# Kernel optimization log

Measured on AMD Instinct MI355X. Metric: run time of the kernel, lower is better.

## Reference

```python
import jax, jax.numpy as jnp
import numpy as np
from math import factorial

# ---- static configuration (matches init_kwargs) ----
IRREPS_IN1 = [(32, 0, 1), (32, 1, -1), (32, 2, 1)]   # (mul, l, parity)
IRREPS_SH  = [(1, 0, 1), (1, 1, -1), (1, 2, 1)]
IRREPS_OUT = [(32, 0, 1), (32, 1, -1), (32, 2, 1)]
NUM_BASIS = 10
HIDDEN = 16
CUTOFF = 4.0
P_ENV = 6  # dimenet envelope_exponent (5) + 1

# ---- real Wigner 3j (Clebsch-Gordan in real SH basis), computed once in numpy ----
def _su2_cg(j1, j2, j3, m1, m2, m3):
    if m3 != m1 + m2:
        return 0.0
    f = factorial
    vmin = max(-j1 + j2 + m3, -j1 + m1, 0)
    vmax = min(j2 + j3 + m1, j3 - j1 + j2, j3 + m3)
    c = (f(2*j3+1) * f(j3+j1-j2) * f(j3-j1+j2) * f(j1+j2-j3) / f(j1+j2+j3+1)
         * f(j3+m3) * f(j3-m3) / (f(j1+m1) * f(j1-m1) * f(j2+m2) * f(j2-m2))) ** 0.5
    s = 0.0
    for v in range(vmin, vmax + 1):
        s += (-1)**(v + j2 + m2) * f(j2+j3+m1-v) * f(j1-m1+v) / (
             f(v) * f(j3-j1+j2-v) * f(j3+m3-v) * f(v+j1-j2-m3))
    return c * s

def _q(l):  # real -> complex SH change of basis
    q = np.zeros((2*l+1, 2*l+1), dtype=complex)
    for m in range(-l, 0):
        q[l+m, l+abs(m)] = 2**-0.5
        q[l+m, l-abs(m)] = -1j * 2**-0.5
    q[l, l] = 1.0
    for m in range(1, l+1):
        q[l+m, l+abs(m)] = (-1)**m * 2**-0.5
        q[l+m, l-abs(m)] = 1j * (-1)**m * 2**-0.5
    return (-1j)**l * q

def _wigner_3j(l1, l2, l3):
    csu2 = np.array([[[ _su2_cg(l1, l2, l3, m1, m2, m3)
                       for m3 in range(-l3, l3+1)]
                      for m2 in range(-l2, l2+1)]
                     for m1 in range(-l1, l1+1)], dtype=complex)
    c = np.einsum('ij,kl,mn,ikm->jln', _q(l1), _q(l2), np.conj(_q(l3)), csu2)
    c = np.real(c)
    n = np.linalg.norm(c)
    return c / n if n > 0 else c

def _slices(irreps):
    s, off = [], 0
    for mul, l, p in irreps:
        d = mul * (2*l + 1)
        s.append((off, off + d))
        off += d
    return s, off

SL1, DIM_IN1 = _slices(IRREPS_IN1)
SL2, DIM_SH = _slices(IRREPS_SH)
SL3, DIM_OUT = _slices(IRREPS_OUT)

_raw = []
for i1, (m1, l1, p1) in enumerate(IRREPS_IN1):
    for i2, (m2, l2, p2) in enumerate(IRREPS_SH):
        for i3, (m3, l3, p3) in enumerate(IRREPS_OUT):
            if p1 * p2 == p3 and abs(l1 - l2) <= l3 <= l1 + l2:
                _raw.append((i1, i2, i3))

_fan = {}
for i1, i2, i3 in _raw:  # path_normalization='element': fan-in per output slot
    _fan[i3] = _fan.get(i3, 0) + IRREPS_IN1[i1][0] * IRREPS_SH[i2][0]

INSTR = []
WEIGHT_NUMEL = 0
for i1, i2, i3 in _raw:
    m1, l1, _ = IRREPS_IN1[i1]
    m2, l2, _ = IRREPS_SH[i2]
    m3, l3, _ = IRREPS_OUT[i3]
    pw = ((2*l3 + 1) / _fan[i3]) ** 0.5  # irrep_normalization='component'
    C = _wigner_3j(l1, l2, l3).astype(np.float32)
    INSTR.append((i1, i2, i3, m1, l1, m2, l2, m3, l3, WEIGHT_NUMEL, pw, C))
    WEIGHT_NUMEL += m1 * m2 * m3

# ---- radial network: Bessel basis (with dimenet envelope) -> Linear -> SiLU -> Linear ----
def _radial(distance, freq, W1, b1, W2, b2):
    d = distance[:, 0]                      # squeeze(-1) -> [E]
    x = (d / CUTOFF)[:, None]               # [E, 1]
    p = P_ENV
    a = -(p + 1) * (p + 2) / 2.0
    b = float(p * (p + 2))
    c = -p * (p + 1) / 2.0
    env = (1.0 / x + a * x**(p-1) + b * x**p + c * x**(p+1)) * (x < 1.0).astype(x.dtype)
    basis = env * jnp.sin(freq * x)         # [E, NUM_BASIS]
    h = jax.nn.silu(basis @ W1 + b1)
    return h @ W2 + b2                      # [E, WEIGHT_NUMEL]

# ---- fully connected tensor product (uvw, external per-edge weights) ----
def _tp(x, sh, weights):
    E = x.shape[0]
    acc = [jnp.zeros((E, m, 2*l + 1), x.dtype) for m, l, _ in IRREPS_OUT]
    for (i1, i2, i3, m1, l1, m2, l2, m3, l3, woff, pw, C) in INSTR:
        a, b = SL1[i1]; xb = x[:, a:b].reshape(E, m1, 2*l1 + 1)
        a, b = SL2[i2]; sb = sh[:, a:b].reshape(E, m2, 2*l2 + 1)
        w = weights[:, woff:woff + m1*m2*m3].reshape(E, m1, m2, m3)
        Cj = jnp.asarray(C)
        acc[i3] = acc[i3] + pw * jnp.einsum('euvw,ijk,eui,evj->ewk', w, Cj, xb, sb)
    return jnp.concatenate([a.reshape(E, -1) for a in acc], axis=1)


def setup_inputs() -> dict:
    key = jax.random.key(0)
    ks = jax.random.split(key, 6)
    E = 16384
    x = jax.random.normal(ks[0], (E, DIM_IN1), jnp.float32)
    rel_pos_sh = jax.random.normal(ks[1], (E, DIM_SH), jnp.float32)
    # distances strictly inside (0, cutoff) so envelope 1/x and mask are benign
    distance = 0.25 + 3.5 * jax.random.uniform(ks[2], (E, 1), jnp.float32)
    freq = jnp.pi * jnp.arange(1, NUM_BASIS + 1, dtype=jnp.float32)
    W1 = 0.4 * jax.random.normal(ks[3], (NUM_BASIS, HIDDEN), jnp.float32)
    b1 = jnp.zeros((HIDDEN,), jnp.float32)
    W2 = 0.1 * jax.random.normal(ks[4], (HIDDEN, WEIGHT_NUMEL), jnp.float32)
    b2 = jnp.zeros((WEIGHT_NUMEL,), jnp.float32)
    return {"x": x, "rel_pos_sh": rel_pos_sh, "distance": distance,
            "freq": freq, "W1": W1, "b1": b1, "W2": W2, "b2": b2}


def reference(x, rel_pos_sh, distance, freq, W1, b1, W2, b2):
    weights = _radial(distance, freq, W1, b1, W2, b2)
    return _tp(x, rel_pos_sh, weights)
```

## Files before the change

### kernel.cpp

```cpp
#include <hip/hip_runtime.h>
#include <cmath>
#include <complex>
#include <cstring>
#include <algorithm>

#define DIM_IN  288
#define DIM_SHD 9
#define NB      10
#define NH      16
#define EPB     16
#define BLOCK   256
#define NINSTR  11
#define XSTR    292
#define ZSTR    164
#define W2B_ELEMS (NINSTR * 32 * 32 * 32)

#define OFF_XO 0
#define OFF_Z  4672
#define OFF_SH 9920
#define POOLSZ 10112

typedef __attribute__((ext_vector_type(8))) short  short8b;
typedef __attribute__((ext_vector_type(4))) float  f32x4;

__device__ float g_C[NINSTR][125];

__device__ __forceinline__ unsigned short f2bf(float f) {
  unsigned int u = __float_as_uint(f);
  unsigned int r = (u + 0x7fffu + ((u >> 16) & 1u)) >> 16;
  return (unsigned short)r;
}

__global__ __launch_bounds__(256) void prep_w2(const float* __restrict__ W2,
                                               const float* __restrict__ b2,
                                               unsigned short* __restrict__ W2b) {
  int gid = blockIdx.x * 256 + threadIdx.x;
  if (gid < W2B_ELEMS) {
    int c = gid >> 5, t = gid & 31;
    float v = (t < 16) ? W2[(size_t)t * 11264 + c] : (t == 16 ? b2[c] : 0.0f);
    W2b[gid] = f2bf(v);
  }
}

template<int INS,int D1,int D2,int D3,int OFF1,int OFF2>
__device__ __forceinline__ void z_phase(
    int tid, const float* __restrict__ s_x,
    const float* __restrict__ s_sh, float* __restrict__ zdst)
{
  const float* __restrict__ Cp = g_C[INS];
  #pragma unroll
  for (int s = 0; s < 2; ++s) {
    int id = tid + s * BLOCK;
    int e = id >> 5, u = id & 31;
    const float* xe = s_x + e * XSTR + OFF1 + u * D1;
    float zk[D3];
    #pragma unroll
    for (int k = 0; k < D3; ++k) zk[k] = 0.f;
    #pragma unroll
    for (int i = 0; i < D1; ++i) {
      float xv = xe[i];
      #pragma unroll
      for (int j = 0; j < D2; ++j) {
        float pr = xv * s_sh[e * 12 + OFF2 + j];
        #pragma unroll
        for (int k = 0; k < D3; ++k)
          zk[k] = fmaf(Cp[(i * D2 + j) * D3 + k], pr, zk[k]);
      }
    }
    #pragma unroll
    for (int k = 0; k < D3; ++k) zdst[e * ZSTR + k * 32 + u] = zk[k];
  }
}

template<int INS,int D3,int SB>
__device__ __forceinline__ void contract(
    int ls, int lq, int a_wt, int b_uh, int my_e,
    const unsigned short* __restrict__ W2b,
    const float* __restrict__ zbuf, short8b hB, float (&acc)[4][9])
{
  const unsigned short* Ap =
      W2b + ((size_t)(INS * 32 + b_uh * 16) * 32 + a_wt * 16 + ls) * 32 + lq * 8;
  const float* zb = zbuf + my_e * ZSTR + b_uh * 16;
  const f32x4 zero4 = {0.f, 0.f, 0.f, 0.f};

  short8b Ra = *(const short8b*)(Ap);
  f32x4 w_cur = __builtin_amdgcn_mfma_f32_16x16x32_bf16(Ra, hB, zero4, 0, 0, 0);
  short8b Rb = *(const short8b*)(Ap + 1024);

  #pragma unroll
  for (int c = 0; c < 4; ++c) {
    float4 zq[D3];
    #pragma unroll
    for (int k = 0; k < D3; ++k)
      zq[k] = *(const float4*)(zb + k * 32 + c * 4);
    #pragma unroll
    for (int i = 0; i < 4; ++i) {
      const int g = c * 4 + i;
      f32x4 w_next;
      if (g < 15) {
        w_next = __builtin_amdgcn_mfma_f32_16x16x32_bf16(Rb, hB, zero4, 0, 0, 0);
        if (g + 2 < 16) Rb = *(const short8b*)(Ap + (size_t)(g + 2) * 1024);
      }
      #pragma unroll
      for (int k = 0; k < D3; ++k) {
        const float zz = (i == 0) ? zq[k].x : (i == 1) ? zq[k].y
                       : (i == 2) ? zq[k].z : zq[k].w;
        acc[0][SB + k] = fmaf(w_cur[0], zz, acc[0][SB + k]);
        acc[1][SB + k] = fmaf(w_cur[1], zz, acc[1][SB + k]);
        acc[2][SB + k] = fmaf(w_cur[2], zz, acc[2][SB + k]);
        acc[3][SB + k] = fmaf(w_cur[3], zz, acc[3][SB + k]);
      }
      if (g < 15) w_cur = w_next;
    }
  }
}

__global__ __launch_bounds__(BLOCK, 2) void conv_kernel(
    const float* __restrict__ xg, const float* __restrict__ shg,
    const float* __restrict__ dist, const float* __restrict__ freq,
    const float* __restrict__ W1, const float* __restrict__ b1,
    const unsigned short* __restrict__ W2b,
    float* __restrict__ out)
{
  __shared__ float s_pool[POOLSZ];
  float* s_xo = s_pool + OFF_XO;
  float* s_z0 = s_pool + OFF_Z;
  float* s_z1 = s_pool + OFF_Z + EPB * ZSTR;
  float* s_sh = s_pool + OFF_SH;
  float* s_basis = s_z1;
  unsigned short* s_hb = (unsigned short*)(s_z1 + 160);

  const int tid = threadIdx.x;
  const int e0 = blockIdx.x * EPB;
  const int l  = tid & 63;
  const int ls = l & 15;
  const int lq = l >> 4;
  const int wid = tid >> 6;
  const int a_wt = wid >> 1;
  const int b_uh = wid & 1;
  const int my_e = ls;

  for (int i4 = tid; i4 < EPB * 72; i4 += BLOCK) {
    int e = i4 / 72, r = i4 - e * 72;
    *(float4*)(s_xo + e * XSTR + r * 4) =
        *(const float4*)(xg + (size_t)(e0 + e) * DIM_IN + r * 4);
  }
  if (tid < EPB * DIM_SHD) {
    int e = tid / DIM_SHD, c = tid - (tid / DIM_SHD) * DIM_SHD;
    s_sh[e * 12 + c] = shg[(size_t)(e0 + e) * DIM_SHD + c];
  }
  if (tid < EPB * NB) {
    int e = tid / NB, n = tid - (tid / NB) * NB;
    float d  = dist[e0 + e];
    float xv = d * 0.25f;
    float x2 = xv * xv, x4 = x2 * x2, x5 = x4 * xv;
    float env = 1.0f / xv + x5 * fmaf(xv, fmaf(xv, -21.0f, 48.0f), -28.0f);
    env = (xv < 1.0f) ? env : 0.0f;
    s_basis[e * NB + n] = env * sinf(freq[n] * xv);
  }
  __syncthreads();

  {
    int e = tid >> 4, t = tid & 15;
    float v = b1[t];
    #pragma unroll
    for (int n = 0; n < NB; ++n) v = fmaf(s_basis[e * NB + n], W1[n * NH + t], v);
    v = v / (1.0f + expf(-v));
    s_hb[e * 32 + t] = f2bf(v);
    s_hb[e * 32 + t + 16] = (t == 0) ? (unsigned short)0x3F80 : (unsigned short)0;
  }
  z_phase< 0, 1, 1, 1,   0, 0>(tid, s_xo, s_sh, s_z0);
  __syncthreads();

  short8b hB = *(const short8b*)(s_hb + my_e * 32 + lq * 8);
  __syncthreads();

  float acc[4][9];
  #pragma unroll
  for (int r = 0; r < 4; ++r)
    #pragma unroll
    for (int a = 0; a < 9; ++a) acc[r][a] = 0.f;

  z_phase< 1, 1, 3, 3,   0, 1>(tid, s_xo, s_sh, s_z1);
  contract< 0, 1, 0>(ls, lq, a_wt, b_uh, my_e, W2b, s_z0, hB, acc);
  __syncthreads();
  z_phase< 2, 1, 5, 5,   0, 4>(tid, s_xo, s_sh, s_z0);
  contract< 1, 3, 1>(ls, lq, a_wt, b_uh, my_e, W2b, s_z1, hB, acc);
  __syncthreads();
  z_phase< 3, 3, 1, 3,  32, 0>(tid, s_xo, s_sh, s_z1);
  contract< 2, 5, 4>(ls, lq, a_wt, b_uh, my_e, W2b, s_z0, hB, acc);
  __syncthreads();
  z_phase< 4, 3, 3, 1,  32, 1>(tid, s_xo, s_sh, s_z0);
  contract< 3, 3, 1>(ls, lq, a_wt, b_uh, my_e, W2b, s_z1, hB, acc);
  __syncthreads();
  z_phase< 5, 3, 3, 5,  32, 1>(tid, s_xo, s_sh, s_z1);
  contract< 4, 1, 0>(ls, lq, a_wt, b_uh, my_e, W2b, s_z0, hB, acc);
  __syncthreads();
  z_phase< 6, 3, 5, 3,  32, 4>(tid, s_xo, s_sh, s_z0);
  contract< 5, 5, 4>(ls, lq, a_wt, b_uh, my_e, W2b, s_z1, hB, acc);
  __syncthreads();
  z_phase< 7, 5, 1, 5, 128, 0>(tid, s_xo, s_sh, s_z1);
  contract< 6, 3, 1>(ls, lq, a_wt, b_uh, my_e, W2b, s_z0, hB, acc);
  __syncthreads();
  z_phase< 8, 5, 3, 3, 128, 1>(tid, s_xo, s_sh, s_z0);
  contract< 7, 5, 4>(ls, lq, a_wt, b_uh, my_e, W2b, s_z1, hB, acc);
  __syncthreads();
  z_phase< 9, 5, 5, 1, 128, 4>(tid, s_xo, s_sh, s_z1);
  contract< 8, 3, 1>(ls, lq, a_wt, b_uh, my_e, W2b, s_z0, hB, acc);
  __syncthreads();
  z_phase<10, 5, 5, 5, 128, 4>(tid, s_xo, s_sh, s_z0);
  contract< 9, 1, 0>(ls, lq, a_wt, b_uh, my_e, W2b, s_z1, hB, acc);
  __syncthreads();
  contract<10, 5, 4>(ls, lq, a_wt, b_uh, my_e, W2b, s_z0, hB, acc);

  __syncthreads();
  if (b_uh == 1) {
    float* row = s_xo + my_e * XSTR;
    #pragma unroll
    for (int r = 0; r < 4; ++r) {
      int w = a_wt * 16 + lq * 4 + r;
      row[w] = acc[r][0];
      #pragma unroll
      for (int k = 0; k < 3; ++k) row[32 + w * 3 + k] = acc[r][1 + k];
      #pragma unroll
      for (int k = 0; k < 5; ++k) row[128 + w * 5 + k] = acc[r][4 + k];
    }
  }
  __syncthreads();
  if (b_uh == 0) {
    float* row = s_xo + my_e * XSTR;
    #pragma unroll
    for (int r = 0; r < 4; ++r) {
      int w = a_wt * 16 + lq * 4 + r;
      row[w] += acc[r][0];
      #pragma unroll
      for (int k = 0; k < 3; ++k) row[32 + w * 3 + k] += acc[r][1 + k];
      #pragma unroll
      for (int k = 0; k < 5; ++k) row[128 + w * 5 + k] += acc[r][4 + k];
    }
  }
  __syncthreads();
  for (int i4 = tid; i4 < EPB * 72; i4 += BLOCK) {
    int e = i4 / 72, r = i4 - e * 72;
    float4 v = *(const float4*)(s_xo + e * XSTR + r * 4);
    *(float4*)(out + (size_t)(e0 + e) * DIM_IN + r * 4) = v;
  }
}

typedef std::complex<double> cd;

static double factd(int n) { double r = 1; for (int i = 2; i <= n; ++i) r *= i; return r; }

static double su2_cg(int j1, int j2, int j3, int m1, int m2, int m3) {
  if (m3 != m1 + m2) return 0.0;
  int vmin = std::max(std::max(-j1 + j2 + m3, -j1 + m1), 0);
  int vmax = std::min(std::min(j2 + j3 + m1, j3 - j1 + j2), j3 + m3);
  if (vmax < vmin) return 0.0;
  double c = std::sqrt(
      factd(2*j3+1) * factd(j3+j1-j2) * factd(j3-j1+j2) * factd(j1+j2-j3) / factd(j1+j2+j3+1)
      * factd(j3+m3) * factd(j3-m3)
      / (factd(j1+m1) * factd(j1-m1) * factd(j2+m2) * factd(j2-m2)));
  double s = 0.0;
  for (int v = vmin; v <= vmax; ++v) {
    double sg = ((v + j2 + m2) & 1) ? -1.0 : 1.0;
    s += sg * factd(j2+j3+m1-v) * factd(j1-m1+v)
         / (factd(v) * factd(j3-j1+j2-v) * factd(j3+m3-v) * factd(v+j1-j2-m3));
  }
  return c * s;
}

static void qmat(int l, cd q[5][5]) {
  for (int a = 0; a < 5; ++a) for (int b = 0; b < 5; ++b) q[a][b] = cd(0, 0);
  const double s = 1.0 / std::sqrt(2.0);
  for (int m = -l; m < 0; ++m) {
    q[l + m][l - m] = cd(s, 0);
    q[l + m][l + m] = cd(0, -s);
  }
  q[l][l] = cd(1, 0);
  for (int m = 1; m <= l; ++m) {
    double sg = (m & 1) ? -1.0 : 1.0;
    q[l + m][l + m] = cd(sg * s, 0);
    q[l + m][l - m] = cd(0, sg * s);
  }
  cd ph = (l == 0) ? cd(1, 0) : (l == 1) ? cd(0, -1) : cd(-1, 0);
  for (int a = 0; a < 5; ++a) for (int b = 0; b < 5; ++b) q[a][b] *= ph;
}

static void wigner3j(int l1, int l2, int l3, double C[5][5][5]) {
  int d1 = 2*l1+1, d2 = 2*l2+1, d3 = 2*l3+1;
  cd q1[5][5], q2[5][5], q3[5][5];
  qmat(l1, q1); qmat(l2, q2); qmat(l3, q3);
  double norm2 = 0;
  for (int j = 0; j < d1; ++j)
    for (int l = 0; l < d2; ++l)
      for (int n = 0; n < d3; ++n) {
        cd sum(0, 0);
        for (int i = 0; i < d1; ++i)
          for (int k = 0; k < d2; ++k)
            for (int m = 0; m < d3; ++m) {
              double cg = su2_cg(l1, l2, l3, i - l1, k - l2, m - l3);
              if (cg != 0.0) sum += q1[i][j] * q2[k][l] * std::conj(q3[m][n]) * cg;
            }
        C[j][l][n] = sum.real();
        norm2 += C[j][l][n] * C[j][l][n];
      }
  double nrm = std::sqrt(norm2);
  if (nrm > 0)
    for (int j = 0; j < d1; ++j)
      for (int l = 0; l < d2; ++l)
        for (int n = 0; n < d3; ++n) C[j][l][n] /= nrm;
}

static void build_C_host(float C_out[NINSTR][125]) {
  const int L1[NINSTR] = {0,0,0,1,1,1,1,2,2,2,2};
  const int L2[NINSTR] = {0,1,2,0,1,1,2,0,1,2,2};
  const int L3[NINSTR] = {0,1,2,1,0,2,1,2,1,0,2};
  std::memset(C_out, 0, sizeof(float) * NINSTR * 125);
  for (int ins = 0; ins < NINSTR; ++ins) {
    int l1 = L1[ins], l2 = L2[ins], l3 = L3[ins];
    int d1 = 2*l1+1, d2 = 2*l2+1, d3 = 2*l3+1;
    double C[5][5][5];
    wigner3j(l1, l2, l3, C);
    double fan = (l3 == 0) ? 96.0 : 128.0;
    double pw = std::sqrt((2*l3+1) / fan);
    for (int i = 0; i < d1; ++i)
      for (int j = 0; j < d2; ++j)
        for (int k = 0; k < d3; ++k)
          C_out[ins][(i * d2 + j) * d3 + k] = (float)(pw * C[i][j][k]);
  }
}

extern "C" void kernel_launch(void* const* d_in, const int* in_sizes, int n_in,
                              void* d_out, int out_size, void* d_ws, size_t ws_size,
                              hipStream_t stream) {
  static float hC[NINSTR][125];
  build_C_host(hC);
  void* dC = nullptr;
  hipGetSymbolAddress(&dC, HIP_SYMBOL(g_C));
  hipMemcpyAsync(dC, hC, sizeof(hC), hipMemcpyHostToDevice, stream);

  const float* xg   = (const float*)d_in[0];
  const float* shg  = (const float*)d_in[1];
  const float* dist = (const float*)d_in[2];
  const float* freq = (const float*)d_in[3];
  const float* W1   = (const float*)d_in[4];
  const float* b1   = (const float*)d_in[5];
  const float* W2   = (const float*)d_in[6];
  const float* b2   = (const float*)d_in[7];
  float* out = (float*)d_out;
  unsigned short* W2b = (unsigned short*)d_ws;

  prep_w2<<<(W2B_ELEMS + 255) / 256, 256, 0, stream>>>(W2, b2, W2b);

  int E = in_sizes[2];
  int blocks = E / EPB;
  conv_kernel<<<blocks, BLOCK, 0, stream>>>(xg, shg, dist, freq, W1, b1, W2b, out);
}
```

Before: 80.58 us.

## Give each wave a private z buffer and drop per-instruction block barriers

Each wave now computes only the half of the z intermediate it consumes, for its own u-half, into a private LDS slice. That removes the shared double-buffered z and the block-wide __syncthreads between the eleven instruction phases. In exchange, the two waves sharing a u-half compute the same z values, so z-phase arithmetic is doubled. The radial basis is also computed inline per thread instead of through an LDS staging step, which drops one barrier but repeats the sin evaluations across threads.

After: 103.6 us. 1.29x slower.

```diff
diff --git a/kernel.cpp b/kernel.cpp
--- a/kernel.cpp
+++ b/kernel.cpp
@@ -12,13 +12,14 @@
 #define BLOCK   256
 #define NINSTR  11
 #define XSTR    292
-#define ZSTR    164
+#define ZW      84
+#define ZBUF    1344
 #define W2B_ELEMS (NINSTR * 32 * 32 * 32)
 
 #define OFF_XO 0
-#define OFF_Z  4672
-#define OFF_SH 9920
-#define POOLSZ 10112
+#define OFF_ZW 4672
+#define OFF_SH 10048
+#define POOLSZ 10240
 
 typedef __attribute__((ext_vector_type(8))) short  short8b;
 typedef __attribute__((ext_vector_type(4))) float  f32x4;
@@ -43,16 +44,16 @@
 }
 
 template<int INS,int D1,int D2,int D3,int OFF1,int OFF2>
-__device__ __forceinline__ void z_phase(
-    int tid, const float* __restrict__ s_x,
-    const float* __restrict__ s_sh, float* __restrict__ zdst)
+__device__ __forceinline__ void z_phase_w(
+    int lane, int b_uh, const float* __restrict__ s_x,
+    const float* __restrict__ s_sh, float* __restrict__ zw)
 {
   const float* __restrict__ Cp = g_C[INS];
   #pragma unroll
-  for (int s = 0; s < 2; ++s) {
-    int id = tid + s * BLOCK;
-    int e = id >> 5, u = id & 31;
-    const float* xe = s_x + e * XSTR + OFF1 + u * D1;
+  for (int s = 0; s < 4; ++s) {
+    int id = lane + s * 64;
+    int e = id >> 4, ul = id & 15;
+    const float* xe = s_x + e * XSTR + OFF1 + (b_uh * 16 + ul) * D1;
     float zk[D3];
     #pragma unroll
     for (int k = 0; k < D3; ++k) zk[k] = 0.f;
@@ -68,19 +69,19 @@
       }
     }
     #pragma unroll
-    for (int k = 0; k < D3; ++k) zdst[e * ZSTR + k * 32 + u] = zk[k];
+    for (int k = 0; k < D3; ++k) zw[e * ZW + k * 16 + ul] = zk[k];
   }
 }
 
 template<int INS,int D3,int SB>
 __device__ __forceinline__ void contract(
-    int ls, int lq, int a_wt, int b_uh, int my_e,
+    int ls, int lq, int a_wt, int b_uh,
     const unsigned short* __restrict__ W2b,
-    const float* __restrict__ zbuf, short8b hB, float (&acc)[4][9])
+    const float* __restrict__ zw, short8b hB, float (&acc)[4][9])
 {
   const unsigned short* Ap =
       W2b + ((size_t)(INS * 32 + b_uh * 16) * 32 + a_wt * 16 + ls) * 32 + lq * 8;
-  const float* zb = zbuf + my_e * ZSTR + b_uh * 16;
+  const float* zb = zw + ls * ZW;
   const f32x4 zero4 = {0.f, 0.f, 0.f, 0.f};
 
   short8b Ra = *(const short8b*)(Ap);
@@ -92,7 +93,7 @@
     float4 zq[D3];
     #pragma unroll
     for (int k = 0; k < D3; ++k)
-      zq[k] = *(const float4*)(zb + k * 32 + c * 4);
+      zq[k] = *(const float4*)(zb + k * 16 + c * 4);
     #pragma unroll
     for (int i = 0; i < 4; ++i) {
       const int g = c * 4 + i;
@@ -124,21 +125,18 @@
 {
   __shared__ float s_pool[POOLSZ];
   float* s_xo = s_pool + OFF_XO;
-  float* s_z0 = s_pool + OFF_Z;
-  float* s_z1 = s_pool + OFF_Z + EPB * ZSTR;
   float* s_sh = s_pool + OFF_SH;
-  float* s_basis = s_z1;
-  unsigned short* s_hb = (unsigned short*)(s_z1 + 160);
 
   const int tid = threadIdx.x;
   const int e0 = blockIdx.x * EPB;
-  const int l  = tid & 63;
-  const int ls = l & 15;
-  const int lq = l >> 4;
+  const int lane = tid & 63;
+  const int ls = lane & 15;
+  const int lq = lane >> 4;
   const int wid = tid >> 6;
   const int a_wt = wid >> 1;
   const int b_uh = wid & 1;
-  const int my_e = ls;
+  float* zw = s_pool + OFF_ZW + wid * ZBUF;
+  unsigned short* s_hb = (unsigned short*)(s_pool + OFF_ZW + 3 * ZBUF);
 
   for (int i4 = tid; i4 < EPB * 72; i4 += BLOCK) {
     int e = i4 / 72, r = i4 - e * 72;
@@ -149,30 +147,25 @@
     int e = tid / DIM_SHD, c = tid - (tid / DIM_SHD) * DIM_SHD;
     s_sh[e * 12 + c] = shg[(size_t)(e0 + e) * DIM_SHD + c];
   }
-  if (tid < EPB * NB) {
-    int e = tid / NB, n = tid - (tid / NB) * NB;
+  __syncthreads();
+
+  {
+    int e = tid >> 4, t = tid & 15;
     float d  = dist[e0 + e];
     float xv = d * 0.25f;
     float x2 = xv * xv, x4 = x2 * x2, x5 = x4 * xv;
     float env = 1.0f / xv + x5 * fmaf(xv, fmaf(xv, -21.0f, 48.0f), -28.0f);
     env = (xv < 1.0f) ? env : 0.0f;
-    s_basis[e * NB + n] = env * sinf(freq[n] * xv);
-  }
-  __syncthreads();
-
-  {
-    int e = tid >> 4, t = tid & 15;
     float v = b1[t];
     #pragma unroll
-    for (int n = 0; n < NB; ++n) v = fmaf(s_basis[e * NB + n], W1[n * NH + t], v);
+    for (int n = 0; n < NB; ++n)
+      v = fmaf(env * sinf(freq[n] * xv), W1[n * NH + t], v);
     v = v / (1.0f + expf(-v));
     s_hb[e * 32 + t] = f2bf(v);
     s_hb[e * 32 + t + 16] = (t == 0) ? (unsigned short)0x3F80 : (unsigned short)0;
   }
-  z_phase< 0, 1, 1, 1,   0, 0>(tid, s_xo, s_sh, s_z0);
-  __syncthreads();
-
-  short8b hB = *(const short8b*)(s_hb + my_e * 32 + lq * 8);
+  __syncthreads();
+  short8b hB = *(const short8b*)(s_hb + ls * 32 + lq * 8);
   __syncthreads();
 
   float acc[4][9];
@@ -181,41 +174,32 @@
     #pragma unroll
     for (int a = 0; a < 9; ++a) acc[r][a] = 0.f;
 
-  z_phase< 1, 1, 3, 3,   0, 1>(tid, s_xo, s_sh, s_z1);
-  contract< 0, 1, 0>(ls, lq, a_wt, b_uh, my_e, W2b, s_z0, hB, acc);
-  __syncthreads();
-  z_phase< 2, 1, 5, 5,   0, 4>(tid, s_xo, s_sh, s_z0);
-  contract< 1, 3, 1>(ls, lq, a_wt, b_uh, my_e, W2b, s_z1, hB, acc);
-  __syncthreads();
-  z_phase< 3, 3, 1, 3,  32, 0>(tid, s_xo, s_sh, s_z1);
-  contract< 2, 5, 4>(ls, lq, a_wt, b_uh, my_e, W2b, s_z0, hB, acc);
-  __syncthreads();
-  z_phase< 4, 3, 3, 1,  32, 1>(tid, s_xo, s_sh, s_z0);
-  contract< 3, 3, 1>(ls, lq, a_wt, b_uh, my_e, W2b, s_z1, hB, acc);
-  __syncthreads();
-  z_phase< 5, 3, 3, 5,  32, 1>(tid, s_xo, s_sh, s_z1);
-  contract< 4, 1, 0>(ls, lq, a_wt, b_uh, my_e, W2b, s_z0, hB, acc);
-  __syncthreads();
-  z_phase< 6, 3, 5, 3,  32, 4>(tid, s_xo, s_sh, s_z0);
-  contract< 5, 5, 4>(ls, lq, a_wt, b_uh, my_e, W2b, s_z1, hB, acc);
-  __syncthreads();
-  z_phase< 7, 5, 1, 5, 128, 0>(tid, s_xo, s_sh, s_z1);
-  contract< 6, 3, 1>(ls, lq, a_wt, b_uh, my_e, W2b, s_z0, hB, acc);
-  __syncthreads();
-  z_phase< 8, 5, 3, 3, 128, 1>(tid, s_xo, s_sh, s_z0);
-  contract< 7, 5, 4>(ls, lq, a_wt, b_uh, my_e, W2b, s_z1, hB, acc);
-  __syncthreads();
-  z_phase< 9, 5, 5, 1, 128, 4>(tid, s_xo, s_sh, s_z1);
-  contract< 8, 3, 1>(ls, lq, a_wt, b_uh, my_e, W2b, s_z0, hB, acc);
-  __syncthreads();
-  z_phase<10, 5, 5, 5, 128, 4>(tid, s_xo, s_sh, s_z0);
-  contract< 9, 1, 0>(ls, lq, a_wt, b_uh, my_e, W2b, s_z1, hB, acc);
-  __syncthreads();
-  contract<10, 5, 4>(ls, lq, a_wt, b_uh, my_e, W2b, s_z0, hB, acc);
+  z_phase_w< 0, 1, 1, 1,   0, 0>(lane, b_uh, s_xo, s_sh, zw);
+  contract< 0, 1, 0>(ls, lq, a_wt, b_uh, W2b, zw, hB, acc);
+  z_phase_w< 1, 1, 3, 3,   0, 1>(lane, b_uh, s_xo, s_sh, zw);
+  contract< 1, 3, 1>(ls, lq, a_wt, b_uh, W2b, zw, hB, acc);
+  z_phase_w< 2, 1, 5, 5,   0, 4>(lane, b_uh, s_xo, s_sh, zw);
+  contract< 2, 5, 4>(ls, lq, a_wt, b_uh, W2b, zw, hB, acc);
+  z_phase_w< 3, 3, 1, 3,  32, 0>(lane, b_uh, s_xo, s_sh, zw);
+  contract< 3, 3, 1>(ls, lq, a_wt, b_uh, W2b, zw, hB, acc);
+  z_phase_w< 4, 3, 3, 1,  32, 1>(lane, b_uh, s_xo, s_sh, zw);
+  contract< 4, 1, 0>(ls, lq, a_wt, b_uh, W2b, zw, hB, acc);
+  z_phase_w< 5, 3, 3, 5,  32, 1>(lane, b_uh, s_xo, s_sh, zw);
+  contract< 5, 5, 4>(ls, lq, a_wt, b_uh, W2b, zw, hB, acc);
+  z_phase_w< 6, 3, 5, 3,  32, 4>(lane, b_uh, s_xo, s_sh, zw);
+  contract< 6, 3, 1>(ls, lq, a_wt, b_uh, W2b, zw, hB, acc);
+  z_phase_w< 7, 5, 1, 5, 128, 0>(lane, b_uh, s_xo, s_sh, zw);
+  contract< 7, 5, 4>(ls, lq, a_wt, b_uh, W2b, zw, hB, acc);
+  z_phase_w< 8, 5, 3, 3, 128, 1>(lane, b_uh, s_xo, s_sh, zw);
+  contract< 8, 3, 1>(ls, lq, a_wt, b_uh, W2b, zw, hB, acc);
+  z_phase_w< 9, 5, 5, 1, 128, 4>(lane, b_uh, s_xo, s_sh, zw);
+  contract< 9, 1, 0>(ls, lq, a_wt, b_uh, W2b, zw, hB, acc);
+  z_phase_w<10, 5, 5, 5, 128, 4>(lane, b_uh, s_xo, s_sh, zw);
+  contract<10, 5, 4>(ls, lq, a_wt, b_uh, W2b, zw, hB, acc);
 
   __syncthreads();
   if (b_uh == 1) {
-    float* row = s_xo + my_e * XSTR;
+    float* row = s_xo + ls * XSTR;
     #pragma unroll
     for (int r = 0; r < 4; ++r) {
       int w = a_wt * 16 + lq * 4 + r;
@@ -228,7 +212,7 @@
   }
   __syncthreads();
   if (b_uh == 0) {
-    float* row = s_xo + my_e * XSTR;
+    float* row = s_xo + ls * XSTR;
     #pragma unroll
     for (int r = 0; r < 4; ++r) {
       int w = a_wt * 16 + lq * 4 + r;
```

## Process 32 edges per block so each W2 fragment load feeds two MFMA tiles

Applied to the files above, without the earlier changes.

Doubles edges per block from 16 to 32. Each weight fragment loaded from global memory now drives two MFMAs, one per 16-edge tile, which halves W2 traffic per edge. The radial basis is also computed inline in the hidden-layer loop instead of through a shared buffer. Accumulator registers double (72 floats per thread) and shared memory roughly doubles, so launch bounds drop to one block per SM. That lowers occupancy and risks register pressure.

New measurement: 109.6 us. 36.0% more time.

```diff
diff --git a/kernel.cpp b/kernel.cpp
--- a/kernel.cpp
+++ b/kernel.cpp
@@ -8,7 +8,7 @@
 #define DIM_SHD 9
 #define NB      10
 #define NH      16
-#define EPB     16
+#define EPB     32
 #define BLOCK   256
 #define NINSTR  11
 #define XSTR    292
@@ -16,9 +16,9 @@
 #define W2B_ELEMS (NINSTR * 32 * 32 * 32)
 
 #define OFF_XO 0
-#define OFF_Z  4672
-#define OFF_SH 9920
-#define POOLSZ 10112
+#define OFF_Z  9344
+#define OFF_SH 19840
+#define POOLSZ 20224
 
 typedef __attribute__((ext_vector_type(8))) short  short8b;
 typedef __attribute__((ext_vector_type(4))) float  f32x4;
@@ -49,7 +49,7 @@
 {
   const float* __restrict__ Cp = g_C[INS];
   #pragma unroll
-  for (int s = 0; s < 2; ++s) {
+  for (int s = 0; s < 4; ++s) {
     int id = tid + s * BLOCK;
     int e = id >> 5, u = id & 31;
     const float* xe = s_x + e * XSTR + OFF1 + u * D1;
@@ -73,49 +73,61 @@
 }
 
 template<int INS,int D3,int SB>
-__device__ __forceinline__ void contract(
-    int ls, int lq, int a_wt, int b_uh, int my_e,
+__device__ __forceinline__ void contract2(
+    int ls, int lq, int a_wt, int b_uh,
     const unsigned short* __restrict__ W2b,
-    const float* __restrict__ zbuf, short8b hB, float (&acc)[4][9])
+    const float* __restrict__ zbuf, short8b hB0, short8b hB1,
+    float (&acc)[2][4][9])
 {
   const unsigned short* Ap =
       W2b + ((size_t)(INS * 32 + b_uh * 16) * 32 + a_wt * 16 + ls) * 32 + lq * 8;
-  const float* zb = zbuf + my_e * ZSTR + b_uh * 16;
+  const float* zb0 = zbuf + ls * ZSTR + b_uh * 16;
+  const float* zb1 = zbuf + (16 + ls) * ZSTR + b_uh * 16;
   const f32x4 zero4 = {0.f, 0.f, 0.f, 0.f};
 
   short8b Ra = *(const short8b*)(Ap);
-  f32x4 w_cur = __builtin_amdgcn_mfma_f32_16x16x32_bf16(Ra, hB, zero4, 0, 0, 0);
+  f32x4 w0_cur = __builtin_amdgcn_mfma_f32_16x16x32_bf16(Ra, hB0, zero4, 0, 0, 0);
+  f32x4 w1_cur = __builtin_amdgcn_mfma_f32_16x16x32_bf16(Ra, hB1, zero4, 0, 0, 0);
   short8b Rb = *(const short8b*)(Ap + 1024);
 
   #pragma unroll
   for (int c = 0; c < 4; ++c) {
-    float4 zq[D3];
-    #pragma unroll
-    for (int k = 0; k < D3; ++k)
-      zq[k] = *(const float4*)(zb + k * 32 + c * 4);
+    float4 zq0[D3], zq1[D3];
+    #pragma unroll
+    for (int k = 0; k < D3; ++k) {
+      zq0[k] = *(const float4*)(zb0 + k * 32 + c * 4);
+      zq1[k] = *(const float4*)(zb1 + k * 32 + c * 4);
+    }
     #pragma unroll
     for (int i = 0; i < 4; ++i) {
       const int g = c * 4 + i;
-      f32x4 w_next;
+      f32x4 w0_next, w1_next;
       if (g < 15) {
-        w_next = __builtin_amdgcn_mfma_f32_16x16x32_bf16(Rb, hB, zero4, 0, 0, 0);
+        w0_next = __builtin_amdgcn_mfma_f32_16x16x32_bf16(Rb, hB0, zero4, 0, 0, 0);
+        w1_next = __builtin_amdgcn_mfma_f32_16x16x32_bf16(Rb, hB1, zero4, 0, 0, 0);
         if (g + 2 < 16) Rb = *(const short8b*)(Ap + (size_t)(g + 2) * 1024);
       }
       #pragma unroll
       for (int k = 0; k < D3; ++k) {
-        const float zz = (i == 0) ? zq[k].x : (i == 1) ? zq[k].y
-                       : (i == 2) ? zq[k].z : zq[k].w;
-        acc[0][SB + k] = fmaf(w_cur[0], zz, acc[0][SB + k]);
-        acc[1][SB + k] = fmaf(w_cur[1], zz, acc[1][SB + k]);
-        acc[2][SB + k] = fmaf(w_cur[2], zz, acc[2][SB + k]);
-        acc[3][SB + k] = fmaf(w_cur[3], zz, acc[3][SB + k]);
-      }
-      if (g < 15) w_cur = w_next;
-    }
-  }
-}
-
-__global__ __launch_bounds__(BLOCK, 2) void conv_kernel(
+        const float z0 = (i == 0) ? zq0[k].x : (i == 1) ? zq0[k].y
+                       : (i == 2) ? zq0[k].z : zq0[k].w;
+        const float z1 = (i == 0) ? zq1[k].x : (i == 1) ? zq1[k].y
+                       : (i == 2) ? zq1[k].z : zq1[k].w;
+        acc[0][0][SB + k] = fmaf(w0_cur[0], z0, acc[0][0][SB + k]);
+        acc[0][1][SB + k] = fmaf(w0_cur[1], z0, acc[0][1][SB + k]);
+        acc[0][2][SB + k] = fmaf(w0_cur[2], z0, acc[0][2][SB + k]);
+        acc[0][3][SB + k] = fmaf(w0_cur[3], z0, acc[0][3][SB + k]);
+        acc[1][0][SB + k] = fmaf(w1_cur[0], z1, acc[1][0][SB + k]);
+        acc[1][1][SB + k] = fmaf(w1_cur[1], z1, acc[1][1][SB + k]);
+        acc[1][2][SB + k] = fmaf(w1_cur[2], z1, acc[1][2][SB + k]);
+        acc[1][3][SB + k] = fmaf(w1_cur[3], z1, acc[1][3][SB + k]);
+      }
+      if (g < 15) { w0_cur = w0_next; w1_cur = w1_next; }
+    }
+  }
+}
+
+__global__ __launch_bounds__(BLOCK, 1) void conv_kernel(
     const float* __restrict__ xg, const float* __restrict__ shg,
     const float* __restrict__ dist, const float* __restrict__ freq,
     const float* __restrict__ W1, const float* __restrict__ b1,
@@ -127,116 +139,119 @@
   float* s_z0 = s_pool + OFF_Z;
   float* s_z1 = s_pool + OFF_Z + EPB * ZSTR;
   float* s_sh = s_pool + OFF_SH;
-  float* s_basis = s_z1;
-  unsigned short* s_hb = (unsigned short*)(s_z1 + 160);
+  unsigned short* s_hb = (unsigned short*)s_z1;
 
   const int tid = threadIdx.x;
   const int e0 = blockIdx.x * EPB;
-  const int l  = tid & 63;
-  const int ls = l & 15;
-  const int lq = l >> 4;
+  const int lane = tid & 63;
+  const int ls = lane & 15;
+  const int lq = lane >> 4;
   const int wid = tid >> 6;
   const int a_wt = wid >> 1;
   const int b_uh = wid & 1;
-  const int my_e = ls;
 
   for (int i4 = tid; i4 < EPB * 72; i4 += BLOCK) {
     int e = i4 / 72, r = i4 - e * 72;
     *(float4*)(s_xo + e * XSTR + r * 4) =
         *(const float4*)(xg + (size_t)(e0 + e) * DIM_IN + r * 4);
   }
-  if (tid < EPB * DIM_SHD) {
-    int e = tid / DIM_SHD, c = tid - (tid / DIM_SHD) * DIM_SHD;
+  for (int i = tid; i < EPB * DIM_SHD; i += BLOCK) {
+    int e = i / DIM_SHD, c = i - (i / DIM_SHD) * DIM_SHD;
     s_sh[e * 12 + c] = shg[(size_t)(e0 + e) * DIM_SHD + c];
   }
-  if (tid < EPB * NB) {
-    int e = tid / NB, n = tid - (tid / NB) * NB;
+  __syncthreads();
+
+  for (int i = tid; i < EPB * NH; i += BLOCK) {
+    int e = i >> 4, t = i & 15;
     float d  = dist[e0 + e];
     float xv = d * 0.25f;
     float x2 = xv * xv, x4 = x2 * x2, x5 = x4 * xv;
     float env = 1.0f / xv + x5 * fmaf(xv, fmaf(xv, -21.0f, 48.0f), -28.0f);
     env = (xv < 1.0f) ? env : 0.0f;
-    s_basis[e * NB + n] = env * sinf(freq[n] * xv);
-  }
-  __syncthreads();
-
-  {
-    int e = tid >> 4, t = tid & 15;
     float v = b1[t];
     #pragma unroll
-    for (int n = 0; n < NB; ++n) v = fmaf(s_basis[e * NB + n], W1[n * NH + t], v);
+    for (int n = 0; n < NB; ++n)
+      v = fmaf(env * sinf(freq[n] * xv), W1[n * NH + t], v);
     v = v / (1.0f + expf(-v));
     s_hb[e * 32 + t] = f2bf(v);
     s_hb[e * 32 + t + 16] = (t == 0) ? (unsigned short)0x3F80 : (unsigned short)0;
   }
   z_phase< 0, 1, 1, 1,   0, 0>(tid, s_xo, s_sh, s_z0);
   __syncthreads();
-
-  short8b hB = *(const short8b*)(s_hb + my_e * 32 + lq * 8);
-  __syncthreads();
-
-  float acc[4][9];
+  short8b hB0 = *(const short8b*)(s_hb + ls * 32 + lq * 8);
+  short8b hB1 = *(const short8b*)(s_hb + (16 + ls) * 32 + lq * 8);
+  __syncthreads();
+
+  float acc[2][4][9];
   #pragma unroll
-  for (int r = 0; r < 4; ++r)
-    #pragma unroll
-    for (int a = 0; a < 9; ++a) acc[r][a] = 0.f;
+  for (int et = 0; et < 2; ++et)
+    #pragma unroll
+    for (int r = 0; r < 4; ++r)
+      #pragma unroll
+      for (int a = 0; a < 9; ++a) acc[et][r][a] = 0.f;
 
   z_phase< 1, 1, 3, 3,   0, 1>(tid, s_xo, s_sh, s_z1);
-  contract< 0, 1, 0>(ls, lq, a_wt, b_uh, my_e, W2b, s_z0, hB, acc);
+  contract2< 0, 1, 0>(ls, lq, a_wt, b_uh, W2b, s_z0, hB0, hB1, acc);
   __syncthreads();
   z_phase< 2, 1, 5, 5,   0, 4>(tid, s_xo, s_sh, s_z0);
-  contract< 1, 3, 1>(ls, lq, a_wt, b_uh, my_e, W2b, s_z1, hB, acc);
+  contract2< 1, 3, 1>(ls, lq, a_wt, b_uh, W2b, s_z1, hB0, hB1, acc);
   __syncthreads();
   z_phase< 3, 3, 1, 3,  32, 0>(tid, s_xo, s_sh, s_z1);
-  contract< 2, 5, 4>(ls, lq, a_wt, b_uh, my_e, W2b, s_z0, hB, acc);
+  contract2< 2, 5, 4>(ls, lq, a_wt, b_uh, W2b, s_z0, hB0, hB1, acc);
   __syncthreads();
   z_phase< 4, 3, 3, 1,  32, 1>(tid, s_xo, s_sh, s_z0);
-  contract< 3, 3, 1>(ls, lq, a_wt, b_uh, my_e, W2b, s_z1, hB, acc);
+  contract2< 3, 3, 1>(ls, lq, a_wt, b_uh, W2b, s_z1, hB0, hB1, acc);
   __syncthreads();
   z_phase< 5, 3, 3, 5,  32, 1>(tid, s_xo, s_sh, s_z1);
-  contract< 4, 1, 0>(ls, lq, a_wt, b_uh, my_e, W2b, s_z0, hB, acc);
+  contract2< 4, 1, 0>(ls, lq, a_wt, b_uh, W2b, s_z0, hB0, hB1, acc);
   __syncthreads();
   z_phase< 6, 3, 5, 3,  32, 4>(tid, s_xo, s_sh, s_z0);
-  contract< 5, 5, 4>(ls, lq, a_wt, b_uh, my_e, W2b, s_z1, hB, acc);
+  contract2< 5, 5, 4>(ls, lq, a_wt, b_uh, W2b, s_z1, hB0, hB1, acc);
   __syncthreads();
   z_phase< 7, 5, 1, 5, 128, 0>(tid, s_xo, s_sh, s_z1);
-  contract< 6, 3, 1>(ls, lq, a_wt, b_uh, my_e, W2b, s_z0, hB, acc);
+  contract2< 6, 3, 1>(ls, lq, a_wt, b_uh, W2b, s_z0, hB0, hB1, acc);
   __syncthreads();
   z_phase< 8, 5, 3, 3, 128, 1>(tid, s_xo, s_sh, s_z0);
-  contract< 7, 5, 4>(ls, lq, a_wt, b_uh, my_e, W2b, s_z1, hB, acc);
+  contract2< 7, 5, 4>(ls, lq, a_wt, b_uh, W2b, s_z1, hB0, hB1, acc);
   __syncthreads();
   z_phase< 9, 5, 5, 1, 128, 4>(tid, s_xo, s_sh, s_z1);
-  contract< 8, 3, 1>(ls, lq, a_wt, b_uh, my_e, W2b, s_z0, hB, acc);
+  contract2< 8, 3, 1>(ls, lq, a_wt, b_uh, W2b, s_z0, hB0, hB1, acc);
   __syncthreads();
   z_phase<10, 5, 5, 5, 128, 4>(tid, s_xo, s_sh, s_z0);
-  contract< 9, 1, 0>(ls, lq, a_wt, b_uh, my_e, W2b, s_z1, hB, acc);
-  __syncthreads();
-  contract<10, 5, 4>(ls, lq, a_wt, b_uh, my_e, W2b, s_z0, hB, acc);
+  contract2< 9, 1, 0>(ls, lq, a_wt, b_uh, W2b, s_z1, hB0, hB1, acc);
+  __syncthreads();
+  contract2<10, 5, 4>(ls, lq, a_wt, b_uh, W2b, s_z0, hB0, hB1, acc);
 
   __syncthreads();
   if (b_uh == 1) {
-    float* row = s_xo + my_e * XSTR;
-    #pragma unroll
-    for (int r = 0; r < 4; ++r) {
-      int w = a_wt * 16 + lq * 4 + r;
-      row[w] = acc[r][0];
-      #pragma unroll
-      for (int k = 0; k < 3; ++k) row[32 + w * 3 + k] = acc[r][1 + k];
-      #pragma unroll
-      for (int k = 0; k < 5; ++k) row[128 + w * 5 + k] = acc[r][4 + k];
+    #pragma unroll
+    for (int et = 0; et < 2; ++et) {
+      float* row = s_xo + (et * 16 + ls) * XSTR;
+      #pragma unroll
+      for (int r = 0; r < 4; ++r) {
+        int w = a_wt * 16 + lq * 4 + r;
+        row[w] = acc[et][r][0];
+        #pragma unroll
+        for (int k = 0; k < 3; ++k) row[32 + w * 3 + k] = acc[et][r][1 + k];
+        #pragma unroll
+        for (int k = 0; k < 5; ++k) row[128 + w * 5 + k] = acc[et][r][4 + k];
+      }
     }
   }
   __syncthreads();
   if (b_uh == 0) {
-    float* row = s_xo + my_e * XSTR;
-    #pragma unroll
-    for (int r = 0; r < 4; ++r) {
-      int w = a_wt * 16 + lq * 4 + r;
-      row[w] += acc[r][0];
-      #pragma unroll
-      for (int k = 0; k < 3; ++k) row[32 + w * 3 + k] += acc[r][1 + k];
-      #pragma unroll
-      for (int k = 0; k < 5; ++k) row[128 + w * 5 + k] += acc[r][4 + k];
+    #pragma unroll
+    for (int et = 0; et < 2; ++et) {
+      float* row = s_xo + (et * 16 + ls) * XSTR;
+      #pragma unroll
+      for (int r = 0; r < 4; ++r) {
+        int w = a_wt * 16 + lq * 4 + r;
+        row[w] += acc[et][r][0];
+        #pragma unroll
+        for (int k = 0; k < 3; ++k) row[32 + w * 3 + k] += acc[et][r][1 + k];
+        #pragma unroll
+        for (int k = 0; k < 5; ++k) row[128 + w * 5 + k] += acc[et][r][4 + k];
+      }
     }
   }
   __syncthreads();
```
